# Kernel tuning notes

Measured on AMD Instinct MI355X. Metric: run time of the kernel, lower is better.

The kernel has to match this reference:

```python
import jax, jax.numpy as jnp
import numpy as np

N_NODES = 100000
N_EDGES = 1600000
IN_CH = 128


def _glorot(key, shape):
    fan_in, fan_out = shape[0], shape[1]
    lim = float(np.sqrt(6.0 / (fan_in + fan_out)))
    return jax.random.uniform(key, shape, jnp.float32, -lim, lim)


def setup_inputs() -> dict:
    key = jax.random.key(0)
    ks = jax.random.split(key, 12)
    x = jax.random.normal(ks[0], (N_NODES, IN_CH), jnp.float32)
    edge_index = jax.random.randint(ks[1], (2, N_EDGES), 0, N_NODES, jnp.int64)
    # conv1: lin2 (in->64), lin1 (2*64 -> 64)
    W2_1 = _glorot(ks[2], (IN_CH, 64)); b2_1 = jnp.zeros((64,), jnp.float32)
    W1_1 = _glorot(ks[3], (128, 64));   b1_1 = jnp.zeros((64,), jnp.float32)
    # conv2: lin2 (64->32), lin1 (2*32 -> 32)
    W2_2 = _glorot(ks[4], (64, 32));    b2_2 = jnp.zeros((32,), jnp.float32)
    W1_2 = _glorot(ks[5], (64, 32));    b1_2 = jnp.zeros((32,), jnp.float32)
    # final lin (32 -> 1)
    Wl = _glorot(ks[6], (32, 1));       bl = jnp.zeros((1,), jnp.float32)
    return {"x": x, "edge_index": edge_index,
            "W2_1": W2_1, "b2_1": b2_1, "W1_1": W1_1, "b1_1": b1_1,
            "W2_2": W2_2, "b2_2": b2_2, "W1_2": W1_2, "b1_2": b1_2,
            "Wl": Wl, "bl": bl}


def _feat_graph_conv(x, src, dst, n, W2, b2, W1, b1):
    # h = lin2(x)
    h = x @ W2 + b2                          # [N, hidden]
    # message: h_j gathered at edge source (edge_weight is None -> identity)
    msg = h[src]                              # [E+N, hidden]
    # scatter-mean aggregation onto destination nodes
    agg = jax.ops.segment_sum(msg, dst, num_segments=n)          # [N, hidden]
    cnt = jax.ops.segment_sum(jnp.ones_like(dst, jnp.float32), dst, num_segments=n)
    agg = agg / jnp.maximum(cnt, 1.0)[:, None]
    # update: lin1(concat(h, agg))
    return jnp.concatenate((h, agg), axis=1) @ W1 + b1


def reference(x, edge_index, W2_1, b2_1, W1_1, b1_1,
              W2_2, b2_2, W1_2, b1_2, Wl, bl):
    n = x.shape[0]
    loops = jnp.arange(n, dtype=edge_index.dtype)
    src = jnp.concatenate((edge_index[0], loops))  # add self loops
    dst = jnp.concatenate((edge_index[1], loops))
    h1 = jax.nn.relu(_feat_graph_conv(x, src, dst, n, W2_1, b2_1, W1_1, b1_1))
    h2 = jax.nn.relu(_feat_graph_conv(h1, src, dst, n, W2_2, b2_2, W1_2, b1_2))
    return h2 @ Wl + bl                       # [N, 1]
```

## Files before the change

kernel.cpp:

```cpp
#include <hip/hip_runtime.h>

#define N_NODES 100000
#define N_EDGES 1600000
constexpr int BLK = 256;
constexpr int NBKT = (N_NODES + 127) / 128;
constexpr int BCAP = 4096;
constexpr int PACK_SHIFT = 17;
constexpr int EPT = 16;
constexpr int EPBLK = BLK * EPT;
constexpr int NSCAT = (N_EDGES + EPBLK - 1) / EPBLK;
constexpr int GTILES = N_NODES / 16;
constexpr int GHALF = GTILES / 2;

__device__ __forceinline__ unsigned short f2bf(float f) {
    unsigned int u = __float_as_uint(f);
    u = (u + 0x7FFFu + ((u >> 16) & 1u)) >> 16;
    return (unsigned short)u;
}
__device__ __forceinline__ float bf2f(unsigned short s) {
    return __uint_as_float(((unsigned int)s) << 16);
}

__global__ void detect_idx64(const unsigned int* __restrict__ e, int* __restrict__ flag) {
    if (blockIdx.x == 0 && threadIdx.x == 0) {
        int is64 = 1;
        for (int i = 0; i < 64; ++i) if (e[2 * i + 1] != 0u) { is64 = 0; break; }
        *flag = is64;
    }
}

__device__ __forceinline__ int load_dst(const int* e, int f, int i) {
    return f ? e[2 * (N_EDGES + i)] : e[N_EDGES + i];
}
__device__ __forceinline__ int load_src(const int* e, int f, int i) {
    return f ? e[2 * i] : e[i];
}

__device__ __forceinline__ void fma_step(float4& acc, float xs, float4 w) {
    acc.x = fmaf(xs, w.x, acc.x);
    acc.y = fmaf(xs, w.y, acc.y);
    acc.z = fmaf(xs, w.z, acc.z);
    acc.w = fmaf(xs, w.w, acc.w);
}
__device__ __forceinline__ void add4(float4& a, float4 v) {
    a.x += v.x; a.y += v.y; a.z += v.z; a.w += v.w;
}
__device__ __forceinline__ void addbf4(float4& a, ushort4 t) {
    a.x += bf2f(t.x); a.y += bf2f(t.y); a.z += bf2f(t.z); a.w += bf2f(t.w);
}


__device__ void scatter_body(const int* __restrict__ eraw, int f,
                             int* __restrict__ cursor, int* __restrict__ ebkt,
                             int bid, void* smem) {
    int* h = (int*)smem;
    const int e0 = bid * EPBLK;
    for (int i = threadIdx.x; i < NBKT; i += BLK) h[i] = 0;
    __syncthreads();
    int bs[EPT], ps[EPT];
#pragma unroll
    for (int k = 0; k < EPT; ++k) {
        const int i = e0 + k * BLK + threadIdx.x;
        if (i < N_EDGES) {
            const int d = load_dst(eraw, f, i);
            const int s = load_src(eraw, f, i);
            bs[k] = d >> 7;
            ps[k] = s | ((d & 127) << PACK_SHIFT);
            atomicAdd(&h[bs[k]], 1);
        } else {
            bs[k] = -1;
            ps[k] = 0;
        }
    }
    __syncthreads();
    for (int b = threadIdx.x; b < NBKT; b += BLK) {
        const int c = h[b];
        if (c) h[b] = atomicAdd(&cursor[b], c);
    }
    __syncthreads();
#pragma unroll
    for (int k = 0; k < EPT; ++k) {
        if (bs[k] >= 0) {
            const int off = atomicAdd(&h[bs[k]], 1);
            ebkt[bs[k] * BCAP + off] = ps[k];
        }
    }
}

__device__ void csrify_body(const int* __restrict__ cnt_b, const int* __restrict__ ebkt,
                            int* __restrict__ adj, int* __restrict__ rowptr,
                            int* __restrict__ deg, int b, void* smem) {
    int* hist = (int*)smem;
    int* excl = hist + 128;
    int* lcur = hist + 256;
    const int s0 = b * BCAP;
    const int s1 = s0 + cnt_b[b];
    for (int i = threadIdx.x; i < 128; i += BLK) hist[i] = 0;
    __syncthreads();
    for (int i = s0 + threadIdx.x; i < s1; i += BLK)
        atomicAdd(&hist[ebkt[i] >> PACK_SHIFT], 1);
    __syncthreads();
    if (threadIdx.x < 128) excl[threadIdx.x] = hist[threadIdx.x];
    __syncthreads();
    for (int off = 1; off < 128; off <<= 1) {
        int t = 0;
        if (threadIdx.x < 128 && threadIdx.x >= off) t = excl[threadIdx.x - off];
        __syncthreads();
        if (threadIdx.x < 128) excl[threadIdx.x] += t;
        __syncthreads();
    }
    if (threadIdx.x < 128) {
        const int e = excl[threadIdx.x] - hist[threadIdx.x];
        lcur[threadIdx.x] = s0 + e;
        const int node = b * 128 + threadIdx.x;
        if (node < N_NODES) {
            rowptr[node] = s0 + e;
            deg[node] = hist[threadIdx.x];
        }
    }
    __syncthreads();
    for (int i = s0 + threadIdx.x; i < s1; i += BLK) {
        const int p = ebkt[i];
        const int pos = atomicAdd(&lcur[p >> PACK_SHIFT], 1);
        adj[pos] = p & ((1 << PACK_SHIFT) - 1);
    }
}

template<int K, int C>
__device__ void gemm_body(const float* __restrict__ X, const float* __restrict__ W,
                          const float* __restrict__ bias, float* __restrict__ Y,
                          unsigned short* __restrict__ Yb, int tile, void* smem) {
    constexpr int CQ = C / 4;
    constexpr int NPB = BLK / CQ;
    constexpr int KQ = K / 4;
    float4* Ws = (float4*)smem;
    float4* xL = Ws + K * CQ;
    for (int i = threadIdx.x; i < K * CQ; i += BLK)
        Ws[i] = reinterpret_cast<const float4*>(W)[i];
    const int cq = threadIdx.x % CQ;
    const int ns = threadIdx.x / CQ;
    const float4 bv = reinterpret_cast<const float4*>(bias)[cq];
    const float4* X4 = reinterpret_cast<const float4*>(X);
    for (int i = threadIdx.x; i < NPB * KQ; i += BLK) {
        const int r = i / KQ;
        const int k4 = i % KQ;
        xL[r * KQ + ((k4 + r) % KQ)] = X4[(size_t)(tile * NPB + r) * KQ + k4];
    }
    __syncthreads();
    const float4* xr = &xL[ns * KQ];
    float4 acc = bv;
#pragma unroll 4
    for (int k4 = 0; k4 < KQ; ++k4) {
        float4 xv = xr[(k4 + ns) % KQ];
        fma_step(acc, xv.x, Ws[(4 * k4 + 0) * CQ + cq]);
        fma_step(acc, xv.y, Ws[(4 * k4 + 1) * CQ + cq]);
        fma_step(acc, xv.z, Ws[(4 * k4 + 2) * CQ + cq]);
        fma_step(acc, xv.w, Ws[(4 * k4 + 3) * CQ + cq]);
    }
    const size_t oi = (size_t)(tile * NPB + ns) * CQ + cq;
    reinterpret_cast<float4*>(Y)[oi] = acc;
    ushort4 bfv;
    bfv.x = f2bf(acc.x); bfv.y = f2bf(acc.y);
    bfv.z = f2bf(acc.z); bfv.w = f2bf(acc.w);
    reinterpret_cast<ushort4*>(Yb)[oi] = bfv;
}

__global__ void scatter_gemm(const int* __restrict__ eraw, const int* __restrict__ flag,
                             int* __restrict__ cursor, int* __restrict__ ebkt,
                             const float* __restrict__ X, const float* __restrict__ W,
                             const float* __restrict__ bias, float* __restrict__ Y,
                             unsigned short* __restrict__ Yb) {
    __shared__ float4 smem[2560];
    if (blockIdx.x < NSCAT) {
        scatter_body(eraw, *flag, cursor, ebkt, blockIdx.x, smem);
    } else {
        gemm_body<128, 64>(X, W, bias, Y, Yb, blockIdx.x - NSCAT, smem);
    }
}

__global__ void csrify_gemm(const int* __restrict__ cnt_b, const int* __restrict__ ebkt,
                            int* __restrict__ adj, int* __restrict__ rowptr,
                            int* __restrict__ deg,
                            const float* __restrict__ X, const float* __restrict__ W,
                            const float* __restrict__ bias, float* __restrict__ Y,
                            unsigned short* __restrict__ Yb) {
    __shared__ float4 smem[2560];
    if (blockIdx.x < NBKT) {
        csrify_body(cnt_b, ebkt, adj, rowptr, deg, blockIdx.x, smem);
    } else {
        gemm_body<128, 64>(X, W, bias, Y, Yb, GHALF + (int)blockIdx.x - NBKT, smem);
    }
}

template<int K, int C>
__global__ void gemm_bias(const float* __restrict__ X, const float* __restrict__ W,
                          const float* __restrict__ bias, float* __restrict__ Y,
                          unsigned short* __restrict__ Yb, int n) {
    constexpr int CQ = C / 4;
    constexpr int NPB = BLK / CQ;
    constexpr int KQ = K / 4;
    __shared__ float4 Ws[K * CQ];
    __shared__ float4 xL[NPB * KQ];
    for (int i = threadIdx.x; i < K * CQ; i += BLK)
        Ws[i] = reinterpret_cast<const float4*>(W)[i];
    const int cq = threadIdx.x % CQ;
    const int ns = threadIdx.x / CQ;
    const float4 bv = reinterpret_cast<const float4*>(bias)[cq];
    const float4* X4 = reinterpret_cast<const float4*>(X);
    const int tile = blockIdx.x;
    for (int i = threadIdx.x; i < NPB * KQ; i += BLK) {
        const int r = i / KQ;
        const int k4 = i % KQ;
        xL[r * KQ + ((k4 + r) % KQ)] = X4[(size_t)(tile * NPB + r) * KQ + k4];
    }
    __syncthreads();
    const float4* xr = &xL[ns * KQ];
    float4 acc = bv;
#pragma unroll 4
    for (int k4 = 0; k4 < KQ; ++k4) {
        float4 xv = xr[(k4 + ns) % KQ];
        fma_step(acc, xv.x, Ws[(4 * k4 + 0) * CQ + cq]);
        fma_step(acc, xv.y, Ws[(4 * k4 + 1) * CQ + cq]);
        fma_step(acc, xv.z, Ws[(4 * k4 + 2) * CQ + cq]);
        fma_step(acc, xv.w, Ws[(4 * k4 + 3) * CQ + cq]);
    }
    const size_t oi = (size_t)(tile * NPB + ns) * CQ + cq;
    reinterpret_cast<float4*>(Y)[oi] = acc;
    ushort4 bfv;
    bfv.x = f2bf(acc.x); bfv.y = f2bf(acc.y);
    bfv.z = f2bf(acc.z); bfv.w = f2bf(acc.w);
    reinterpret_cast<ushort4*>(Yb)[oi] = bfv;
}

template<int KH, int C, int TPB>
__global__ void update_gather(const float* __restrict__ P,
                              const unsigned short* __restrict__ Pb,
                              const int* __restrict__ rowptr, const int* __restrict__ cnt,
                              const int* __restrict__ adj,
                              const float* __restrict__ W, const float* __restrict__ bias,
                              float* __restrict__ Y, int n) {
    constexpr int CQ = C / 4;
    constexpr int NPB = TPB / CQ;
    constexpr int K = 2 * KH;
    __shared__ float4 Ws[K * CQ];
    __shared__ float4 Ag[NPB][CQ + 1];
    for (int i = threadIdx.x; i < K * CQ; i += TPB)
        Ws[i] = reinterpret_cast<const float4*>(W)[i];
    __syncthreads();
    const int cq = threadIdx.x % CQ;
    const int ns = threadIdx.x / CQ;
    const float4 bv = reinterpret_cast<const float4*>(bias)[cq];
    const float4* P4 = reinterpret_cast<const float4*>(P);
    const ushort4* Pb4 = reinterpret_cast<const ushort4*>(Pb);
    const int node = blockIdx.x * NPB + ns;
    const int start = rowptr[node];
    const int deg = cnt[node];
    const float inv = 1.0f / (float)(deg + 1);
    const float4* pr = &P4[(size_t)node * CQ];

    float4 agg = {0.f, 0.f, 0.f, 0.f};
    int j = 0;
    for (; j + 7 < deg; j += 8) {
        const int s0 = adj[start + j];
        const int s1 = adj[start + j + 1];
        const int s2 = adj[start + j + 2];
        const int s3 = adj[start + j + 3];
        const int s4 = adj[start + j + 4];
        const int s5 = adj[start + j + 5];
        const int s6 = adj[start + j + 6];
        const int s7 = adj[start + j + 7];
        const ushort4 t0 = Pb4[(size_t)s0 * CQ + cq];
        const ushort4 t1 = Pb4[(size_t)s1 * CQ + cq];
        const ushort4 t2 = Pb4[(size_t)s2 * CQ + cq];
        const ushort4 t3 = Pb4[(size_t)s3 * CQ + cq];
        const ushort4 t4 = Pb4[(size_t)s4 * CQ + cq];
        const ushort4 t5 = Pb4[(size_t)s5 * CQ + cq];
        const ushort4 t6 = Pb4[(size_t)s6 * CQ + cq];
        const ushort4 t7 = Pb4[(size_t)s7 * CQ + cq];
        addbf4(agg, t0); addbf4(agg, t1); addbf4(agg, t2); addbf4(agg, t3);
        addbf4(agg, t4); addbf4(agg, t5); addbf4(agg, t6); addbf4(agg, t7);
    }
    if (j + 3 < deg) {
        const int s0 = adj[start + j];
        const int s1 = adj[start + j + 1];
        const int s2 = adj[start + j + 2];
        const int s3 = adj[start + j + 3];
        const ushort4 t0 = Pb4[(size_t)s0 * CQ + cq];
        const ushort4 t1 = Pb4[(size_t)s1 * CQ + cq];
        const ushort4 t2 = Pb4[(size_t)s2 * CQ + cq];
        const ushort4 t3 = Pb4[(size_t)s3 * CQ + cq];
        addbf4(agg, t0); addbf4(agg, t1); addbf4(agg, t2); addbf4(agg, t3);
        j += 4;
    }
    for (; j < deg; ++j)
        addbf4(agg, Pb4[(size_t)adj[start + j] * CQ + cq]);

    float4 acc = bv;
#pragma unroll 4
    for (int k4 = 0; k4 < KH / 4; ++k4) {
        float4 pv = pr[k4];
        fma_step(acc, pv.x, Ws[(4 * k4 + 0) * CQ + cq]);
        fma_step(acc, pv.y, Ws[(4 * k4 + 1) * CQ + cq]);
        fma_step(acc, pv.z, Ws[(4 * k4 + 2) * CQ + cq]);
        fma_step(acc, pv.w, Ws[(4 * k4 + 3) * CQ + cq]);
    }
    {
        float4 pv = pr[cq];
        add4(agg, pv);
        agg.x *= inv; agg.y *= inv; agg.z *= inv; agg.w *= inv;
    }
    Ag[ns][cq] = agg;
    __syncthreads();
#pragma unroll 4
    for (int k4 = 0; k4 < KH / 4; ++k4) {
        float4 av = Ag[ns][k4];
        fma_step(acc, av.x, Ws[(KH + 4 * k4 + 0) * CQ + cq]);
        fma_step(acc, av.y, Ws[(KH + 4 * k4 + 1) * CQ + cq]);
        fma_step(acc, av.z, Ws[(KH + 4 * k4 + 2) * CQ + cq]);
        fma_step(acc, av.w, Ws[(KH + 4 * k4 + 3) * CQ + cq]);
    }
    acc.x = fmaxf(acc.x, 0.0f);
    acc.y = fmaxf(acc.y, 0.0f);
    acc.z = fmaxf(acc.z, 0.0f);
    acc.w = fmaxf(acc.w, 0.0f);
    reinterpret_cast<float4*>(Y)[(size_t)node * CQ + cq] = acc;
}

__global__ void update2_final(const float* __restrict__ P,
                              const unsigned short* __restrict__ Pb,
                              const int* __restrict__ rowptr, const int* __restrict__ cnt,
                              const int* __restrict__ adj,
                              const float* __restrict__ W, const float* __restrict__ bias,
                              const float* __restrict__ Wl, const float* __restrict__ bl,
                              float* __restrict__ out, int n) {
    constexpr int CQ = 8;
    constexpr int NPB = BLK / CQ;
    __shared__ float4 Ws[64 * CQ];
    __shared__ float4 Ag[NPB][CQ + 1];
    for (int i = threadIdx.x; i < 64 * CQ; i += BLK)
        Ws[i] = reinterpret_cast<const float4*>(W)[i];
    __syncthreads();
    const int cq = threadIdx.x % CQ;
    const int ns = threadIdx.x / CQ;
    const float4 bv = reinterpret_cast<const float4*>(bias)[cq];
    const float4 wlv = reinterpret_cast<const float4*>(Wl)[cq];
    const float blv = bl[0];
    const float4* P4 = reinterpret_cast<const float4*>(P);
    const ushort4* Pb4 = reinterpret_cast<const ushort4*>(Pb);
    const int node = blockIdx.x * NPB + ns;
    const int start = rowptr[node];
    const int deg = cnt[node];
    const float inv = 1.0f / (float)(deg + 1);
    const float4* pr = &P4[(size_t)node * CQ];

    float4 agg = {0.f, 0.f, 0.f, 0.f};
    int j = 0;
    for (; j + 7 < deg; j += 8) {
        const int s0 = adj[start + j];
        const int s1 = adj[start + j + 1];
        const int s2 = adj[start + j + 2];
        const int s3 = adj[start + j + 3];
        const int s4 = adj[start + j + 4];
        const int s5 = adj[start + j + 5];
        const int s6 = adj[start + j + 6];
        const int s7 = adj[start + j + 7];
        const ushort4 t0 = Pb4[(size_t)s0 * CQ + cq];
        const ushort4 t1 = Pb4[(size_t)s1 * CQ + cq];
        const ushort4 t2 = Pb4[(size_t)s2 * CQ + cq];
        const ushort4 t3 = Pb4[(size_t)s3 * CQ + cq];
        const ushort4 t4 = Pb4[(size_t)s4 * CQ + cq];
        const ushort4 t5 = Pb4[(size_t)s5 * CQ + cq];
        const ushort4 t6 = Pb4[(size_t)s6 * CQ + cq];
        const ushort4 t7 = Pb4[(size_t)s7 * CQ + cq];
        addbf4(agg, t0); addbf4(agg, t1); addbf4(agg, t2); addbf4(agg, t3);
        addbf4(agg, t4); addbf4(agg, t5); addbf4(agg, t6); addbf4(agg, t7);
    }
    if (j + 3 < deg) {
        const int s0 = adj[start + j];
        const int s1 = adj[start + j + 1];
        const int s2 = adj[start + j + 2];
        const int s3 = adj[start + j + 3];
        const ushort4 t0 = Pb4[(size_t)s0 * CQ + cq];
        const ushort4 t1 = Pb4[(size_t)s1 * CQ + cq];
        const ushort4 t2 = Pb4[(size_t)s2 * CQ + cq];
        const ushort4 t3 = Pb4[(size_t)s3 * CQ + cq];
        addbf4(agg, t0); addbf4(agg, t1); addbf4(agg, t2); addbf4(agg, t3);
        j += 4;
    }
    for (; j < deg; ++j)
        addbf4(agg, Pb4[(size_t)adj[start + j] * CQ + cq]);

    float4 acc = bv;
#pragma unroll
    for (int k4 = 0; k4 < 8; ++k4) {
        float4 pv = pr[k4];
        fma_step(acc, pv.x, Ws[(4 * k4 + 0) * CQ + cq]);
        fma_step(acc, pv.y, Ws[(4 * k4 + 1) * CQ + cq]);
        fma_step(acc, pv.z, Ws[(4 * k4 + 2) * CQ + cq]);
        fma_step(acc, pv.w, Ws[(4 * k4 + 3) * CQ + cq]);
    }
    {
        float4 pv = pr[cq];
        add4(agg, pv);
        agg.x *= inv; agg.y *= inv; agg.z *= inv; agg.w *= inv;
    }
    Ag[ns][cq] = agg;
    __syncthreads();
#pragma unroll
    for (int k4 = 0; k4 < 8; ++k4) {
        float4 av = Ag[ns][k4];
        fma_step(acc, av.x, Ws[(32 + 4 * k4 + 0) * CQ + cq]);
        fma_step(acc, av.y, Ws[(32 + 4 * k4 + 1) * CQ + cq]);
        fma_step(acc, av.z, Ws[(32 + 4 * k4 + 2) * CQ + cq]);
        fma_step(acc, av.w, Ws[(32 + 4 * k4 + 3) * CQ + cq]);
    }
    float v = fmaxf(acc.x, 0.0f) * wlv.x + fmaxf(acc.y, 0.0f) * wlv.y
            + fmaxf(acc.z, 0.0f) * wlv.z + fmaxf(acc.w, 0.0f) * wlv.w;
    v += __shfl_xor(v, 4, 8);
    v += __shfl_xor(v, 2, 8);
    v += __shfl_xor(v, 1, 8);
    if (cq == 0) out[node] = v + blv;
}

extern "C" void kernel_launch(void* const* d_in, const int* in_sizes, int n_in,
                              void* d_out, int out_size, void* d_ws, size_t ws_size,
                              hipStream_t stream) {
    const float* x    = (const float*)d_in[0];
    const int*   eraw = (const int*)d_in[1];
    const float* W2_1 = (const float*)d_in[2];
    const float* b2_1 = (const float*)d_in[3];
    const float* W1_1 = (const float*)d_in[4];
    const float* b1_1 = (const float*)d_in[5];
    const float* W2_2 = (const float*)d_in[6];
    const float* b2_2 = (const float*)d_in[7];
    const float* W1_2 = (const float*)d_in[8];
    const float* b1_2 = (const float*)d_in[9];
    const float* Wl   = (const float*)d_in[10];
    const float* bl   = (const float*)d_in[11];
    float* out = (float*)d_out;

    char* ws = (char*)d_ws;
    int* flag   = (int*)ws;
    size_t off = 256;
    int* cursor = (int*)(ws + off); off += sizeof(int) * (size_t)(NBKT + 2);
    off = (off + 255) & ~(size_t)255;
    int* ebkt   = (int*)(ws + off); off += sizeof(int) * (size_t)NBKT * BCAP;
    off = (off + 255) & ~(size_t)255;
    int* adj    = (int*)(ws + off); off += sizeof(int) * (size_t)NBKT * BCAP;
    int* rowptr = (int*)(ws + off); off += sizeof(int) * (size_t)N_NODES;
    int* deg    = (int*)(ws + off); off += sizeof(int) * (size_t)N_NODES;
    off = (off + 255) & ~(size_t)255;
    float* bufA = (float*)(ws + off); off += sizeof(float) * (size_t)N_NODES * 64;
    float* bufC = (float*)(ws + off); off += sizeof(float) * (size_t)N_NODES * 64;
    unsigned short* bufAb = (unsigned short*)(ws + off);
    off += sizeof(unsigned short) * (size_t)N_NODES * 64;

    hipMemsetAsync(cursor, 0, sizeof(int) * (size_t)(NBKT + 2), stream);

    detect_idx64<<<1, 64, 0, stream>>>((const unsigned int*)eraw, flag);

    scatter_gemm<<<NSCAT + GHALF, BLK, 0, stream>>>(eraw, flag, cursor, ebkt,
                                                    x, W2_1, b2_1, bufA, bufAb);
    csrify_gemm<<<NBKT + GHALF, BLK, 0, stream>>>(cursor, ebkt, adj, rowptr, deg,
                                                  x, W2_1, b2_1, bufA, bufAb);

    update_gather<64, 64, 512><<<N_NODES / 32, 512, 0, stream>>>(bufA, bufAb, rowptr, deg, adj, W1_1, b1_1, bufC, N_NODES);

    gemm_bias<64, 32><<<N_NODES / 32, BLK, 0, stream>>>(bufC, W2_2, b2_2, bufA, bufAb, N_NODES);
    update2_final<<<N_NODES / 32, BLK, 0, stream>>>(bufA, bufAb, rowptr, deg, adj, W1_2, b1_2, Wl, bl, out, N_NODES);
}
```

Measured before the change: 187.0 us.

## Widen layer-1 gather to 16-byte loads with 8 threads per node

```diff
diff --git a/kernel.cpp b/kernel.cpp
--- a/kernel.cpp
+++ b/kernel.cpp
@@ -19,6 +19,12 @@
 }
 __device__ __forceinline__ float bf2f(unsigned short s) {
     return __uint_as_float(((unsigned int)s) << 16);
+}
+__device__ __forceinline__ float bflo(unsigned int u) {
+    return __uint_as_float(u << 16);
+}
+__device__ __forceinline__ float bfhi(unsigned int u) {
+    return __uint_as_float(u & 0xffff0000u);
 }
 
 __global__ void detect_idx64(const unsigned int* __restrict__ e, int* __restrict__ flag) {
@@ -232,24 +238,142 @@
     reinterpret_cast<ushort4*>(Yb)[oi] = bfv;
 }
 
-template<int KH, int C, int TPB>
-__global__ void update_gather(const float* __restrict__ P,
+template<int TPB>
+__global__ void update_gather_w(const float* __restrict__ P,
+                                const unsigned short* __restrict__ Pb,
+                                const int* __restrict__ rowptr, const int* __restrict__ cnt,
+                                const int* __restrict__ adj,
+                                const float* __restrict__ W, const float* __restrict__ bias,
+                                float* __restrict__ Y, int n) {
+    constexpr int CQ = 8;
+    constexpr int NPB = TPB / CQ;
+    constexpr int QROW = 16;
+    constexpr int K = 128;
+    __shared__ float4 Ws[K * QROW];
+    __shared__ float4 Ag[NPB][QROW + 1];
+    for (int i = threadIdx.x; i < K * QROW; i += TPB)
+        Ws[i] = reinterpret_cast<const float4*>(W)[i];
+    __syncthreads();
+    const int cq = threadIdx.x & 7;
+    const int ns = threadIdx.x >> 3;
+    const int nodeRaw = blockIdx.x * NPB + ns;
+    const bool active = nodeRaw < n;
+    const int node = active ? nodeRaw : (n - 1);
+    const int start = rowptr[node];
+    const int deg = cnt[node];
+    const float inv = 1.0f / (float)(deg + 1);
+    const float4* pr = reinterpret_cast<const float4*>(P) + (size_t)node * QROW;
+    const uint4* Pb16 = reinterpret_cast<const uint4*>(Pb);
+
+    float ag0 = 0.f, ag1 = 0.f, ag2 = 0.f, ag3 = 0.f;
+    float ag4 = 0.f, ag5 = 0.f, ag6 = 0.f, ag7 = 0.f;
+    const int dmain = deg & ~7;
+    int j = 0;
+    for (; j < dmain; j += 8) {
+        const int idx = adj[start + j + cq];
+        const int s0 = __shfl(idx, 0, 8);
+        const int s1 = __shfl(idx, 1, 8);
+        const int s2 = __shfl(idx, 2, 8);
+        const int s3 = __shfl(idx, 3, 8);
+        const int s4 = __shfl(idx, 4, 8);
+        const int s5 = __shfl(idx, 5, 8);
+        const int s6 = __shfl(idx, 6, 8);
+        const int s7 = __shfl(idx, 7, 8);
+        const uint4 t0 = Pb16[(size_t)s0 * 8 + cq];
+        const uint4 t1 = Pb16[(size_t)s1 * 8 + cq];
+        const uint4 t2 = Pb16[(size_t)s2 * 8 + cq];
+        const uint4 t3 = Pb16[(size_t)s3 * 8 + cq];
+        const uint4 t4 = Pb16[(size_t)s4 * 8 + cq];
+        const uint4 t5 = Pb16[(size_t)s5 * 8 + cq];
+        const uint4 t6 = Pb16[(size_t)s6 * 8 + cq];
+        const uint4 t7 = Pb16[(size_t)s7 * 8 + cq];
+#define ACC(t) do { \
+        ag0 += bflo((t).x); ag1 += bfhi((t).x); \
+        ag2 += bflo((t).y); ag3 += bfhi((t).y); \
+        ag4 += bflo((t).z); ag5 += bfhi((t).z); \
+        ag6 += bflo((t).w); ag7 += bfhi((t).w); } while (0)
+        ACC(t0); ACC(t1); ACC(t2); ACC(t3);
+        ACC(t4); ACC(t5); ACC(t6); ACC(t7);
+    }
+    if (j < deg) {
+        const int rem = deg - j;
+        const int idx = (cq < rem) ? adj[start + j + cq] : 0;
+        for (int k = 0; k < rem; ++k) {
+            const int s = __shfl(idx, k, 8);
+            const uint4 t = Pb16[(size_t)s * 8 + cq];
+            ACC(t);
+        }
+    }
+#undef ACC
+
+    float4 acc0 = reinterpret_cast<const float4*>(bias)[2 * cq];
+    float4 acc1 = reinterpret_cast<const float4*>(bias)[2 * cq + 1];
+#pragma unroll 4
+    for (int k4 = 0; k4 < QROW; ++k4) {
+        const float4 pv = pr[k4];
+        fma_step(acc0, pv.x, Ws[(4 * k4 + 0) * QROW + 2 * cq]);
+        fma_step(acc1, pv.x, Ws[(4 * k4 + 0) * QROW + 2 * cq + 1]);
+        fma_step(acc0, pv.y, Ws[(4 * k4 + 1) * QROW + 2 * cq]);
+        fma_step(acc1, pv.y, Ws[(4 * k4 + 1) * QROW + 2 * cq + 1]);
+        fma_step(acc0, pv.z, Ws[(4 * k4 + 2) * QROW + 2 * cq]);
+        fma_step(acc1, pv.z, Ws[(4 * k4 + 2) * QROW + 2 * cq + 1]);
+        fma_step(acc0, pv.w, Ws[(4 * k4 + 3) * QROW + 2 * cq]);
+        fma_step(acc1, pv.w, Ws[(4 * k4 + 3) * QROW + 2 * cq + 1]);
+    }
+    {
+        const float4 pv0 = pr[2 * cq];
+        const float4 pv1 = pr[2 * cq + 1];
+        float4 a0, a1;
+        a0.x = (ag0 + pv0.x) * inv; a0.y = (ag1 + pv0.y) * inv;
+        a0.z = (ag2 + pv0.z) * inv; a0.w = (ag3 + pv0.w) * inv;
+        a1.x = (ag4 + pv1.x) * inv; a1.y = (ag5 + pv1.y) * inv;
+        a1.z = (ag6 + pv1.z) * inv; a1.w = (ag7 + pv1.w) * inv;
+        Ag[ns][2 * cq] = a0;
+        Ag[ns][2 * cq + 1] = a1;
+    }
+    __syncthreads();
+#pragma unroll 4
+    for (int k4 = 0; k4 < QROW; ++k4) {
+        const float4 av = Ag[ns][k4];
+        fma_step(acc0, av.x, Ws[(64 + 4 * k4 + 0) * QROW + 2 * cq]);
+        fma_step(acc1, av.x, Ws[(64 + 4 * k4 + 0) * QROW + 2 * cq + 1]);
+        fma_step(acc0, av.y, Ws[(64 + 4 * k4 + 1) * QROW + 2 * cq]);
+        fma_step(acc1, av.y, Ws[(64 + 4 * k4 + 1) * QROW + 2 * cq + 1]);
+        fma_step(acc0, av.z, Ws[(64 + 4 * k4 + 2) * QROW + 2 * cq]);
+        fma_step(acc1, av.z, Ws[(64 + 4 * k4 + 2) * QROW + 2 * cq + 1]);
+        fma_step(acc0, av.w, Ws[(64 + 4 * k4 + 3) * QROW + 2 * cq]);
+        fma_step(acc1, av.w, Ws[(64 + 4 * k4 + 3) * QROW + 2 * cq + 1]);
+    }
+    acc0.x = fmaxf(acc0.x, 0.f); acc0.y = fmaxf(acc0.y, 0.f);
+    acc0.z = fmaxf(acc0.z, 0.f); acc0.w = fmaxf(acc0.w, 0.f);
+    acc1.x = fmaxf(acc1.x, 0.f); acc1.y = fmaxf(acc1.y, 0.f);
+    acc1.z = fmaxf(acc1.z, 0.f); acc1.w = fmaxf(acc1.w, 0.f);
+    if (active) {
+        float4* Y4 = reinterpret_cast<float4*>(Y) + (size_t)nodeRaw * QROW;
+        Y4[2 * cq] = acc0;
+        Y4[2 * cq + 1] = acc1;
+    }
+}
+
+__global__ void update2_final(const float* __restrict__ P,
                               const unsigned short* __restrict__ Pb,
                               const int* __restrict__ rowptr, const int* __restrict__ cnt,
                               const int* __restrict__ adj,
                               const float* __restrict__ W, const float* __restrict__ bias,
-                              float* __restrict__ Y, int n) {
-    constexpr int CQ = C / 4;
-    constexpr int NPB = TPB / CQ;
-    constexpr int K = 2 * KH;
-    __shared__ float4 Ws[K * CQ];
+                              const float* __restrict__ Wl, const float* __restrict__ bl,
+                              float* __restrict__ out, int n) {
+    constexpr int CQ = 8;
+    constexpr int NPB = BLK / CQ;
+    __shared__ float4 Ws[64 * CQ];
     __shared__ float4 Ag[NPB][CQ + 1];
-    for (int i = threadIdx.x; i < K * CQ; i += TPB)
+    for (int i = threadIdx.x; i < 64 * CQ; i += BLK)
         Ws[i] = reinterpret_cast<const float4*>(W)[i];
     __syncthreads();
     const int cq = threadIdx.x % CQ;
     const int ns = threadIdx.x / CQ;
     const float4 bv = reinterpret_cast<const float4*>(bias)[cq];
+    const float4 wlv = reinterpret_cast<const float4*>(Wl)[cq];
+    const float blv = bl[0];
     const float4* P4 = reinterpret_cast<const float4*>(P);
     const ushort4* Pb4 = reinterpret_cast<const ushort4*>(Pb);
     const int node = blockIdx.x * NPB + ns;
@@ -296,101 +420,6 @@
         addbf4(agg, Pb4[(size_t)adj[start + j] * CQ + cq]);
 
     float4 acc = bv;
-#pragma unroll 4
-    for (int k4 = 0; k4 < KH / 4; ++k4) {
-        float4 pv = pr[k4];
-        fma_step(acc, pv.x, Ws[(4 * k4 + 0) * CQ + cq]);
-        fma_step(acc, pv.y, Ws[(4 * k4 + 1) * CQ + cq]);
-        fma_step(acc, pv.z, Ws[(4 * k4 + 2) * CQ + cq]);
-        fma_step(acc, pv.w, Ws[(4 * k4 + 3) * CQ + cq]);
-    }
-    {
-        float4 pv = pr[cq];
-        add4(agg, pv);
-        agg.x *= inv; agg.y *= inv; agg.z *= inv; agg.w *= inv;
-    }
-    Ag[ns][cq] = agg;
-    __syncthreads();
-#pragma unroll 4
-    for (int k4 = 0; k4 < KH / 4; ++k4) {
-        float4 av = Ag[ns][k4];
-        fma_step(acc, av.x, Ws[(KH + 4 * k4 + 0) * CQ + cq]);
-        fma_step(acc, av.y, Ws[(KH + 4 * k4 + 1) * CQ + cq]);
-        fma_step(acc, av.z, Ws[(KH + 4 * k4 + 2) * CQ + cq]);
-        fma_step(acc, av.w, Ws[(KH + 4 * k4 + 3) * CQ + cq]);
-    }
-    acc.x = fmaxf(acc.x, 0.0f);
-    acc.y = fmaxf(acc.y, 0.0f);
-    acc.z = fmaxf(acc.z, 0.0f);
-    acc.w = fmaxf(acc.w, 0.0f);
-    reinterpret_cast<float4*>(Y)[(size_t)node * CQ + cq] = acc;
-}
-
-__global__ void update2_final(const float* __restrict__ P,
-                              const unsigned short* __restrict__ Pb,
-                              const int* __restrict__ rowptr, const int* __restrict__ cnt,
-                              const int* __restrict__ adj,
-                              const float* __restrict__ W, const float* __restrict__ bias,
-                              const float* __restrict__ Wl, const float* __restrict__ bl,
-                              float* __restrict__ out, int n) {
-    constexpr int CQ = 8;
-    constexpr int NPB = BLK / CQ;
-    __shared__ float4 Ws[64 * CQ];
-    __shared__ float4 Ag[NPB][CQ + 1];
-    for (int i = threadIdx.x; i < 64 * CQ; i += BLK)
-        Ws[i] = reinterpret_cast<const float4*>(W)[i];
-    __syncthreads();
-    const int cq = threadIdx.x % CQ;
-    const int ns = threadIdx.x / CQ;
-    const float4 bv = reinterpret_cast<const float4*>(bias)[cq];
-    const float4 wlv = reinterpret_cast<const float4*>(Wl)[cq];
-    const float blv = bl[0];
-    const float4* P4 = reinterpret_cast<const float4*>(P);
-    const ushort4* Pb4 = reinterpret_cast<const ushort4*>(Pb);
-    const int node = blockIdx.x * NPB + ns;
-    const int start = rowptr[node];
-    const int deg = cnt[node];
-    const float inv = 1.0f / (float)(deg + 1);
-    const float4* pr = &P4[(size_t)node * CQ];
-
-    float4 agg = {0.f, 0.f, 0.f, 0.f};
-    int j = 0;
-    for (; j + 7 < deg; j += 8) {
-        const int s0 = adj[start + j];
-        const int s1 = adj[start + j + 1];
-        const int s2 = adj[start + j + 2];
-        const int s3 = adj[start + j + 3];
-        const int s4 = adj[start + j + 4];
-        const int s5 = adj[start + j + 5];
-        const int s6 = adj[start + j + 6];
-        const int s7 = adj[start + j + 7];
-        const ushort4 t0 = Pb4[(size_t)s0 * CQ + cq];
-        const ushort4 t1 = Pb4[(size_t)s1 * CQ + cq];
-        const ushort4 t2 = Pb4[(size_t)s2 * CQ + cq];
-        const ushort4 t3 = Pb4[(size_t)s3 * CQ + cq];
-        const ushort4 t4 = Pb4[(size_t)s4 * CQ + cq];
-        const ushort4 t5 = Pb4[(size_t)s5 * CQ + cq];
-        const ushort4 t6 = Pb4[(size_t)s6 * CQ + cq];
-        const ushort4 t7 = Pb4[(size_t)s7 * CQ + cq];
-        addbf4(agg, t0); addbf4(agg, t1); addbf4(agg, t2); addbf4(agg, t3);
-        addbf4(agg, t4); addbf4(agg, t5); addbf4(agg, t6); addbf4(agg, t7);
-    }
-    if (j + 3 < deg) {
-        const int s0 = adj[start + j];
-        const int s1 = adj[start + j + 1];
-        const int s2 = adj[start + j + 2];
-        const int s3 = adj[start + j + 3];
-        const ushort4 t0 = Pb4[(size_t)s0 * CQ + cq];
-        const ushort4 t1 = Pb4[(size_t)s1 * CQ + cq];
-        const ushort4 t2 = Pb4[(size_t)s2 * CQ + cq];
-        const ushort4 t3 = Pb4[(size_t)s3 * CQ + cq];
-        addbf4(agg, t0); addbf4(agg, t1); addbf4(agg, t2); addbf4(agg, t3);
-        j += 4;
-    }
-    for (; j < deg; ++j)
-        addbf4(agg, Pb4[(size_t)adj[start + j] * CQ + cq]);
-
-    float4 acc = bv;
 #pragma unroll
     for (int k4 = 0; k4 < 8; ++k4) {
         float4 pv = pr[k4];
@@ -464,7 +493,8 @@
     csrify_gemm<<<NBKT + GHALF, BLK, 0, stream>>>(cursor, ebkt, adj, rowptr, deg,
                                                   x, W2_1, b2_1, bufA, bufAb);
 
-    update_gather<64, 64, 512><<<N_NODES / 32, 512, 0, stream>>>(bufA, bufAb, rowptr, deg, adj, W1_1, b1_1, bufC, N_NODES);
+    update_gather_w<512><<<(N_NODES + 63) / 64, 512, 0, stream>>>(
+        bufA, bufAb, rowptr, deg, adj, W1_1, b1_1, bufC, N_NODES);
 
     gemm_bias<64, 32><<<N_NODES / 32, BLK, 0, stream>>>(bufC, W2_2, b2_2, bufA, bufAb, N_NODES);
     update2_final<<<N_NODES / 32, BLK, 0, stream>>>(bufA, bufAb, rowptr, deg, adj, W1_2, b1_2, Wl, bl, out, N_NODES);
```

After: 187.7 us. No clear change (+0.4%).
